# Optimization experiments

Measured on AMD Instinct MI355X. Metric: run time of the kernel, lower is better.

## Reference

```python
import jax, jax.numpy as jnp
import numpy as np

B, D, O, E = 8192, 1024, 1024, 8

def setup_inputs() -> dict:
    key = jax.random.key(0)
    ks = jax.random.split(key, 5)
    s = 1.0 / np.sqrt(D)
    return {
        "x": jax.random.normal(ks[0], (B, D), dtype=jnp.float32),
        "Wg": jax.random.uniform(ks[1], (D, E), jnp.float32, -s, s),
        "bg": jax.random.uniform(ks[2], (E,), jnp.float32, -s, s),
        "We": jax.random.uniform(ks[3], (E, D, O), jnp.float32, -s, s),
        "be": jax.random.uniform(ks[4], (E, O), jnp.float32, -s, s),
    }

def reference(x, Wg, bg, We, be):
    # gating: [B, E], softmax over experts (dim=1)
    gates = jax.nn.softmax(x @ Wg + bg, axis=1)
    # dense expert outputs: [B, E, O] (single batched GEMM over all experts)
    expert_out = jnp.einsum('bd,edo->beo', x, We) + be[None, :, :]
    # softmax-weighted combine (bmm of [B,1,E] @ [B,E,O] -> [B,O])
    return jnp.einsum('be,beo->bo', gates, expert_out)
```

## Files before the change

### kernel.cpp

```cpp
#include <hip/hip_runtime.h>
#include <hip/hip_bf16.h>
#include <stdint.h>

#define B_SZ 8192
#define D_SZ 1024
#define O_SZ 1024
#define E_SZ 8

typedef __bf16 bf16_t;
typedef __bf16 bf16x8 __attribute__((ext_vector_type(8)));
typedef __bf16 bf16x4 __attribute__((ext_vector_type(4)));
typedef float  f32x4  __attribute__((ext_vector_type(4)));

__global__ __launch_bounds__(256) void gating_kernel(
    const float* __restrict__ x, const float* __restrict__ Wg,
    const float* __restrict__ bg, float* __restrict__ gates) {
  const int w = threadIdx.x >> 6, lane = threadIdx.x & 63;
  const int b = blockIdx.x * 4 + w;
  const float* xr = x + (size_t)b * D_SZ;
  float acc[8];
#pragma unroll
  for (int e = 0; e < 8; ++e) acc[e] = 0.f;
  for (int it = 0; it < 16; ++it) {
    int d = it * 64 + lane;
    float xv = xr[d];
    const float4* wr = (const float4*)(Wg + d * 8);
    float4 w0 = wr[0], w1 = wr[1];
    acc[0] += xv * w0.x; acc[1] += xv * w0.y;
    acc[2] += xv * w0.z; acc[3] += xv * w0.w;
    acc[4] += xv * w1.x; acc[5] += xv * w1.y;
    acc[6] += xv * w1.z; acc[7] += xv * w1.w;
  }
#pragma unroll
  for (int off = 32; off >= 1; off >>= 1) {
#pragma unroll
    for (int e = 0; e < 8; ++e) acc[e] += __shfl_xor(acc[e], off, 64);
  }
  if (lane == 0) {
#pragma unroll
    for (int e = 0; e < 8; ++e) acc[e] += bg[e];
    float m = acc[0];
#pragma unroll
    for (int e = 1; e < 8; ++e) m = fmaxf(m, acc[e]);
    float s = 0.f, ex[8];
#pragma unroll
    for (int e = 0; e < 8; ++e) { ex[e] = __expf(acc[e] - m); s += ex[e]; }
    float inv = 1.0f / s;
    float* gr = gates + (size_t)b * 8;
#pragma unroll
    for (int e = 0; e < 8; ++e) gr[e] = ex[e] * inv;
  }
}

__global__ __launch_bounds__(256) void cvt_x_kernel(
    const float* __restrict__ x, bf16_t* __restrict__ xb) {
  size_t i = (size_t)blockIdx.x * 256 + threadIdx.x;
  float4 v = ((const float4*)x)[i];
  bf16x4 o;
  o[0] = (bf16_t)v.x; o[1] = (bf16_t)v.y; o[2] = (bf16_t)v.z; o[3] = (bf16_t)v.w;
  ((bf16x4*)xb)[i] = o;
}

__global__ __launch_bounds__(256) void transpose_we(
    const float* __restrict__ We, bf16_t* __restrict__ WeT) {
  __shared__ float tile[64][65];
  const int e = blockIdx.z;
  const int d0 = blockIdx.y * 64, o0 = blockIdx.x * 64;
  const int tx = threadIdx.x & 63, ty = threadIdx.x >> 6;
  const float* src = We + (size_t)e * D_SZ * O_SZ;
#pragma unroll
  for (int i = 0; i < 16; ++i) {
    int d = ty + i * 4;
    tile[d][tx] = src[(size_t)(d0 + d) * O_SZ + o0 + tx];
  }
  __syncthreads();
  bf16_t* dst = WeT + (size_t)e * O_SZ * D_SZ;
#pragma unroll
  for (int i = 0; i < 16; ++i) {
    int o = ty + i * 4;
    dst[(size_t)(o0 + o) * D_SZ + d0 + tx] = (bf16_t)tile[tx][o];
  }
}

__device__ __forceinline__ void gload_lds16(const bf16_t* g, char* l) {
  __builtin_amdgcn_global_load_lds(
      (const __attribute__((address_space(1))) void*)g,
      (__attribute__((address_space(3))) void*)l, 16, 0, 0);
}

__global__ __launch_bounds__(256, 2) void moe_gemm(
    const bf16_t* __restrict__ xb,
    const bf16_t* __restrict__ wet,
    const float* __restrict__ gates,
    const float* __restrict__ be,
    float* __restrict__ out)
{
  __shared__ bf16_t lA[128 * 32];
  __shared__ bf16_t lB[128 * 32];
  __shared__ float  lG[128 * 8];

  const int tid = threadIdx.x;
  const int b0 = blockIdx.y * 128;
  const int o0 = blockIdx.x * 128;

  {
    const float* gsrc = gates + (size_t)b0 * 8;
#pragma unroll
    for (int i = 0; i < 4; ++i) lG[tid + 256 * i] = gsrc[tid + 256 * i];
  }

  const int w = tid >> 6;
  const int lane = tid & 63;
  const int wm = (w >> 1) * 64;
  const int wn = (w & 1) * 64;
  const int m16 = lane & 15;
  const int q = lane >> 4;

  const int gi0 = tid, gi1 = tid + 256;
  const int ar0 = gi0 >> 2, ac0 = (((gi0 & 3) ^ ((gi0 >> 3) & 3)) * 8);
  const int ar1 = gi1 >> 2, ac1 = (((gi1 & 3) ^ ((gi1 >> 3) & 3)) * 8);
  char* lA0 = (char*)lA + w * 64 * 16;
  char* lA1 = (char*)lA + (256 + w * 64) * 16;
  char* lB0 = (char*)lB + w * 64 * 16;
  char* lB1 = (char*)lB + (256 + w * 64) * 16;

  const bf16_t* Abase = xb + (size_t)b0 * D_SZ;

  f32x4 outAcc[4][4];
#pragma unroll
  for (int i = 0; i < 4; ++i)
#pragma unroll
    for (int j = 0; j < 4; ++j) outAcc[i][j] = f32x4{0.f, 0.f, 0.f, 0.f};

  for (int e = 0; e < E_SZ; ++e) {
    const bf16_t* Bbase = wet + ((size_t)e * O_SZ + o0) * D_SZ;
    f32x4 acc[4][4];
#pragma unroll
    for (int i = 0; i < 4; ++i)
#pragma unroll
      for (int j = 0; j < 4; ++j) acc[i][j] = f32x4{0.f, 0.f, 0.f, 0.f};

    for (int kt = 0; kt < D_SZ / 32; ++kt) {
      const int kc = kt * 32;
      __syncthreads();
      gload_lds16(Abase + (size_t)ar0 * D_SZ + kc + ac0, lA0);
      gload_lds16(Abase + (size_t)ar1 * D_SZ + kc + ac1, lA1);
      gload_lds16(Bbase + (size_t)ar0 * D_SZ + kc + ac0, lB0);
      gload_lds16(Bbase + (size_t)ar1 * D_SZ + kc + ac1, lB1);
      __syncthreads();

      bf16x8 af[4], bf[4];
#pragma unroll
      for (int i = 0; i < 4; ++i) {
        int r = wm + i * 16 + m16;
        int pg = (q ^ ((r >> 1) & 3)) * 8;
        af[i] = *(const bf16x8*)&lA[r * 32 + pg];
      }
#pragma unroll
      for (int j = 0; j < 4; ++j) {
        int r = wn + j * 16 + m16;
        int pg = (q ^ ((r >> 1) & 3)) * 8;
        bf[j] = *(const bf16x8*)&lB[r * 32 + pg];
      }
#pragma unroll
      for (int i = 0; i < 4; ++i)
#pragma unroll
        for (int j = 0; j < 4; ++j)
          acc[i][j] = __builtin_amdgcn_mfma_f32_16x16x32_bf16(
              af[i], bf[j], acc[i][j], 0, 0, 0);
    }

#pragma unroll
    for (int j = 0; j < 4; ++j) {
      float bec = be[e * O_SZ + o0 + wn + j * 16 + m16];
#pragma unroll
      for (int i = 0; i < 4; ++i) {
#pragma unroll
        for (int rg = 0; rg < 4; ++rg) {
          float gv = lG[(wm + i * 16 + q * 4 + rg) * 8 + e];
          outAcc[i][j][rg] += gv * (acc[i][j][rg] + bec);
        }
      }
    }
  }

#pragma unroll
  for (int i = 0; i < 4; ++i)
#pragma unroll
    for (int rg = 0; rg < 4; ++rg) {
      float* orow = out + (size_t)(b0 + wm + i * 16 + q * 4 + rg) * O_SZ
                    + o0 + wn + m16;
#pragma unroll
      for (int j = 0; j < 4; ++j) orow[j * 16] = outAcc[i][j][rg];
    }
}

extern "C" void kernel_launch(void* const* d_in, const int* in_sizes, int n_in,
                              void* d_out, int out_size, void* d_ws, size_t ws_size,
                              hipStream_t stream) {
  const float* x  = (const float*)d_in[0];
  const float* Wg = (const float*)d_in[1];
  const float* bg = (const float*)d_in[2];
  const float* We = (const float*)d_in[3];
  const float* be = (const float*)d_in[4];
  float* out = (float*)d_out;

  char* ws = (char*)d_ws;
  float*  gates = (float*)ws;
  bf16_t* xb    = (bf16_t*)(ws + (1 << 18));
  bf16_t* wet   = (bf16_t*)(ws + (1 << 18) + (1 << 24));

  gating_kernel<<<B_SZ / 4, 256, 0, stream>>>(x, Wg, bg, gates);
  cvt_x_kernel<<<(B_SZ * D_SZ) / (4 * 256), 256, 0, stream>>>(x, xb);
  transpose_we<<<dim3(O_SZ / 64, D_SZ / 64, E_SZ), 256, 0, stream>>>(We, wet);
  moe_gemm<<<dim3(O_SZ / 128, B_SZ / 128), 256, 0, stream>>>(xb, wet, gates, be, out);
}
```

Before: 300.7 us.

## Split expert loop across two grid slices and fuse x conversion into gating

The expert loop in the MoE GEMM is split over a third grid dimension of two, so each block handles four experts and writes a partial result. A combine kernel then adds the partials. This doubles the block count (512 to 1024) to fill more compute units, at the cost of an extra 32MB write plus a read-add pass. Separately, the bf16 conversion of x is fused into the gating kernel so x is read once, which also removes one launch.

```diff
diff --git a/kernel.cpp b/kernel.cpp
--- a/kernel.cpp
+++ b/kernel.cpp
@@ -12,24 +12,35 @@
 typedef __bf16 bf16x4 __attribute__((ext_vector_type(4)));
 typedef float  f32x4  __attribute__((ext_vector_type(4)));
 
-__global__ __launch_bounds__(256) void gating_kernel(
+__global__ __launch_bounds__(256) void gating_cvt_kernel(
     const float* __restrict__ x, const float* __restrict__ Wg,
-    const float* __restrict__ bg, float* __restrict__ gates) {
+    const float* __restrict__ bg, float* __restrict__ gates,
+    bf16_t* __restrict__ xb) {
   const int w = threadIdx.x >> 6, lane = threadIdx.x & 63;
   const int b = blockIdx.x * 4 + w;
   const float* xr = x + (size_t)b * D_SZ;
+  bf16_t* xbr = xb + (size_t)b * D_SZ;
   float acc[8];
 #pragma unroll
   for (int e = 0; e < 8; ++e) acc[e] = 0.f;
-  for (int it = 0; it < 16; ++it) {
-    int d = it * 64 + lane;
-    float xv = xr[d];
-    const float4* wr = (const float4*)(Wg + d * 8);
-    float4 w0 = wr[0], w1 = wr[1];
-    acc[0] += xv * w0.x; acc[1] += xv * w0.y;
-    acc[2] += xv * w0.z; acc[3] += xv * w0.w;
-    acc[4] += xv * w1.x; acc[5] += xv * w1.y;
-    acc[6] += xv * w1.z; acc[7] += xv * w1.w;
+#pragma unroll
+  for (int it = 0; it < 4; ++it) {
+    const int d = it * 256 + lane * 4;
+    float4 xv = *(const float4*)(xr + d);
+    bf16x4 ov;
+    ov[0] = (bf16_t)xv.x; ov[1] = (bf16_t)xv.y;
+    ov[2] = (bf16_t)xv.z; ov[3] = (bf16_t)xv.w;
+    *(bf16x4*)(xbr + d) = ov;
+    const float xs[4] = {xv.x, xv.y, xv.z, xv.w};
+#pragma unroll
+    for (int j = 0; j < 4; ++j) {
+      const float4* wr = (const float4*)(Wg + (size_t)(d + j) * 8);
+      float4 w0 = wr[0], w1 = wr[1];
+      acc[0] += xs[j] * w0.x; acc[1] += xs[j] * w0.y;
+      acc[2] += xs[j] * w0.z; acc[3] += xs[j] * w0.w;
+      acc[4] += xs[j] * w1.x; acc[5] += xs[j] * w1.y;
+      acc[6] += xs[j] * w1.z; acc[7] += xs[j] * w1.w;
+    }
   }
 #pragma unroll
   for (int off = 32; off >= 1; off >>= 1) {
@@ -50,15 +61,6 @@
 #pragma unroll
     for (int e = 0; e < 8; ++e) gr[e] = ex[e] * inv;
   }
-}
-
-__global__ __launch_bounds__(256) void cvt_x_kernel(
-    const float* __restrict__ x, bf16_t* __restrict__ xb) {
-  size_t i = (size_t)blockIdx.x * 256 + threadIdx.x;
-  float4 v = ((const float4*)x)[i];
-  bf16x4 o;
-  o[0] = (bf16_t)v.x; o[1] = (bf16_t)v.y; o[2] = (bf16_t)v.z; o[3] = (bf16_t)v.w;
-  ((bf16x4*)xb)[i] = o;
 }
 
 __global__ __launch_bounds__(256) void transpose_we(
@@ -93,7 +95,8 @@
     const bf16_t* __restrict__ wet,
     const float* __restrict__ gates,
     const float* __restrict__ be,
-    float* __restrict__ out)
+    float* __restrict__ out,
+    float* __restrict__ part1)
 {
   __shared__ bf16_t lA[128 * 32];
   __shared__ bf16_t lB[128 * 32];
@@ -102,6 +105,10 @@
   const int tid = threadIdx.x;
   const int b0 = blockIdx.y * 128;
   const int o0 = blockIdx.x * 128;
+  const int ngrp = gridDim.z;
+  const int ne = E_SZ / ngrp;
+  const int e0 = blockIdx.z * ne;
+  float* __restrict__ dst = blockIdx.z ? part1 : out;
 
   {
     const float* gsrc = gates + (size_t)b0 * 8;
@@ -132,7 +139,8 @@
 #pragma unroll
     for (int j = 0; j < 4; ++j) outAcc[i][j] = f32x4{0.f, 0.f, 0.f, 0.f};
 
-  for (int e = 0; e < E_SZ; ++e) {
+  for (int ei = 0; ei < ne; ++ei) {
+    const int e = e0 + ei;
     const bf16_t* Bbase = wet + ((size_t)e * O_SZ + o0) * D_SZ;
     f32x4 acc[4][4];
 #pragma unroll
@@ -149,7 +157,7 @@
       gload_lds16(Bbase + (size_t)ar1 * D_SZ + kc + ac1, lB1);
       __syncthreads();
 
-      bf16x8 af[4], bf[4];
+      bf16x8 af[4], bfr[4];
 #pragma unroll
       for (int i = 0; i < 4; ++i) {
         int r = wm + i * 16 + m16;
@@ -160,14 +168,14 @@
       for (int j = 0; j < 4; ++j) {
         int r = wn + j * 16 + m16;
         int pg = (q ^ ((r >> 1) & 3)) * 8;
-        bf[j] = *(const bf16x8*)&lB[r * 32 + pg];
+        bfr[j] = *(const bf16x8*)&lB[r * 32 + pg];
       }
 #pragma unroll
       for (int i = 0; i < 4; ++i)
 #pragma unroll
         for (int j = 0; j < 4; ++j)
           acc[i][j] = __builtin_amdgcn_mfma_f32_16x16x32_bf16(
-              af[i], bf[j], acc[i][j], 0, 0, 0);
+              af[i], bfr[j], acc[i][j], 0, 0, 0);
     }
 
 #pragma unroll
@@ -188,11 +196,20 @@
   for (int i = 0; i < 4; ++i)
 #pragma unroll
     for (int rg = 0; rg < 4; ++rg) {
-      float* orow = out + (size_t)(b0 + wm + i * 16 + q * 4 + rg) * O_SZ
+      float* orow = dst + (size_t)(b0 + wm + i * 16 + q * 4 + rg) * O_SZ
                     + o0 + wn + m16;
 #pragma unroll
       for (int j = 0; j < 4; ++j) orow[j * 16] = outAcc[i][j][rg];
     }
+}
+
+__global__ __launch_bounds__(256) void combine_kernel(
+    float* __restrict__ out, const float* __restrict__ p1) {
+  size_t i = (size_t)blockIdx.x * 256 + threadIdx.x;
+  float4 a = ((const float4*)out)[i];
+  float4 b = ((const float4*)p1)[i];
+  a.x += b.x; a.y += b.y; a.z += b.z; a.w += b.w;
+  ((float4*)out)[i] = a;
 }
 
 extern "C" void kernel_launch(void* const* d_in, const int* in_sizes, int n_in,
@@ -209,9 +226,20 @@
   float*  gates = (float*)ws;
   bf16_t* xb    = (bf16_t*)(ws + (1 << 18));
   bf16_t* wet   = (bf16_t*)(ws + (1 << 18) + (1 << 24));
-
-  gating_kernel<<<B_SZ / 4, 256, 0, stream>>>(x, Wg, bg, gates);
-  cvt_x_kernel<<<(B_SZ * D_SZ) / (4 * 256), 256, 0, stream>>>(x, xb);
+  float*  p1    = (float*)(ws + (1 << 18) + 2 * (size_t)(1 << 24));
+
+  const size_t need = (size_t)(1 << 18) + 2 * (size_t)(1 << 24)
+                    + (size_t)B_SZ * O_SZ * sizeof(float);
+  const bool split = ws_size >= need;
+
+  gating_cvt_kernel<<<B_SZ / 4, 256, 0, stream>>>(x, Wg, bg, gates, xb);
   transpose_we<<<dim3(O_SZ / 64, D_SZ / 64, E_SZ), 256, 0, stream>>>(We, wet);
-  moe_gemm<<<dim3(O_SZ / 128, B_SZ / 128), 256, 0, stream>>>(xb, wet, gates, be, out);
-}
+  if (split) {
+    moe_gemm<<<dim3(O_SZ / 128, B_SZ / 128, 2), 256, 0, stream>>>(
+        xb, wet, gates, be, out, p1);
+    combine_kernel<<<(B_SZ * O_SZ / 4) / 256, 256, 0, stream>>>(out, p1);
+  } else {
+    moe_gemm<<<dim3(O_SZ / 128, B_SZ / 128, 1), 256, 0, stream>>>(
+        xb, wet, gates, be, out, p1);
+  }
+}
```

Result: slower. 333.2 us (+10.8%).

## Fuse gating, x conversion and We transpose into one prep kernel

Applied to the files above, without the earlier changes.

Merges the three preprocessing kernels into a single launch that splits its blocks between gating-plus-bf16-conversion of x and transposing/converting We. The gating path reads x once with float4 loads and reuses it for the bf16 store, removing a second full read of x. The transpose now uses float4 loads and bf16x8 stores. This cuts launch overhead and redundant traffic, but the two block roles now share one shared-memory footprint, and the transpose's tile reads with a large stride may cause LDS bank conflicts.

```diff
diff --git a/kernel.cpp b/kernel.cpp
--- a/kernel.cpp
+++ b/kernel.cpp
@@ -12,73 +12,91 @@
 typedef __bf16 bf16x4 __attribute__((ext_vector_type(4)));
 typedef float  f32x4  __attribute__((ext_vector_type(4)));
 
-__global__ __launch_bounds__(256) void gating_kernel(
+__global__ __launch_bounds__(256) void prep_kernel(
     const float* __restrict__ x, const float* __restrict__ Wg,
-    const float* __restrict__ bg, float* __restrict__ gates) {
-  const int w = threadIdx.x >> 6, lane = threadIdx.x & 63;
-  const int b = blockIdx.x * 4 + w;
-  const float* xr = x + (size_t)b * D_SZ;
-  float acc[8];
-#pragma unroll
-  for (int e = 0; e < 8; ++e) acc[e] = 0.f;
-  for (int it = 0; it < 16; ++it) {
-    int d = it * 64 + lane;
-    float xv = xr[d];
-    const float4* wr = (const float4*)(Wg + d * 8);
-    float4 w0 = wr[0], w1 = wr[1];
-    acc[0] += xv * w0.x; acc[1] += xv * w0.y;
-    acc[2] += xv * w0.z; acc[3] += xv * w0.w;
-    acc[4] += xv * w1.x; acc[5] += xv * w1.y;
-    acc[6] += xv * w1.z; acc[7] += xv * w1.w;
-  }
-#pragma unroll
-  for (int off = 32; off >= 1; off >>= 1) {
-#pragma unroll
-    for (int e = 0; e < 8; ++e) acc[e] += __shfl_xor(acc[e], off, 64);
-  }
-  if (lane == 0) {
-#pragma unroll
-    for (int e = 0; e < 8; ++e) acc[e] += bg[e];
-    float m = acc[0];
-#pragma unroll
-    for (int e = 1; e < 8; ++e) m = fmaxf(m, acc[e]);
-    float s = 0.f, ex[8];
-#pragma unroll
-    for (int e = 0; e < 8; ++e) { ex[e] = __expf(acc[e] - m); s += ex[e]; }
+    const float* __restrict__ bg, const float* __restrict__ We,
+    float* __restrict__ gates, bf16_t* __restrict__ xb,
+    bf16_t* __restrict__ WeT) {
+  __shared__ float tile[64][65];
+  const int tid = threadIdx.x;
+  if (blockIdx.x < 2048) {
+    const int w = tid >> 6, lane = tid & 63;
+    const int b = blockIdx.x * 4 + w;
+    const float* xr = x + (size_t)b * D_SZ;
+    float acc[8];
+#pragma unroll
+    for (int e = 0; e < 8; ++e) acc[e] = 0.f;
+    float xs[16];
+#pragma unroll
+    for (int it = 0; it < 4; ++it) {
+      const int d = it * 256 + lane * 4;
+      float4 xv = *(const float4*)(xr + d);
+      xs[it * 4 + 0] = xv.x; xs[it * 4 + 1] = xv.y;
+      xs[it * 4 + 2] = xv.z; xs[it * 4 + 3] = xv.w;
+#pragma unroll
+      for (int j = 0; j < 4; ++j) {
+        const float4* wr = (const float4*)(Wg + (size_t)(d + j) * 8);
+        float4 w0 = wr[0], w1 = wr[1];
+        float xj = xs[it * 4 + j];
+        acc[0] += xj * w0.x; acc[1] += xj * w0.y;
+        acc[2] += xj * w0.z; acc[3] += xj * w0.w;
+        acc[4] += xj * w1.x; acc[5] += xj * w1.y;
+        acc[6] += xj * w1.z; acc[7] += xj * w1.w;
+      }
+    }
+#pragma unroll
+    for (int off = 32; off >= 1; off >>= 1) {
+#pragma unroll
+      for (int e = 0; e < 8; ++e) acc[e] += __shfl_xor(acc[e], off, 64);
+    }
+    float g[8];
+#pragma unroll
+    for (int e = 0; e < 8; ++e) g[e] = acc[e] + bg[e];
+    float m = g[0];
+#pragma unroll
+    for (int e = 1; e < 8; ++e) m = fmaxf(m, g[e]);
+    float s = 0.f;
+#pragma unroll
+    for (int e = 0; e < 8; ++e) { g[e] = __expf(g[e] - m); s += g[e]; }
     float inv = 1.0f / s;
-    float* gr = gates + (size_t)b * 8;
-#pragma unroll
-    for (int e = 0; e < 8; ++e) gr[e] = ex[e] * inv;
-  }
-}
-
-__global__ __launch_bounds__(256) void cvt_x_kernel(
-    const float* __restrict__ x, bf16_t* __restrict__ xb) {
-  size_t i = (size_t)blockIdx.x * 256 + threadIdx.x;
-  float4 v = ((const float4*)x)[i];
-  bf16x4 o;
-  o[0] = (bf16_t)v.x; o[1] = (bf16_t)v.y; o[2] = (bf16_t)v.z; o[3] = (bf16_t)v.w;
-  ((bf16x4*)xb)[i] = o;
-}
-
-__global__ __launch_bounds__(256) void transpose_we(
-    const float* __restrict__ We, bf16_t* __restrict__ WeT) {
-  __shared__ float tile[64][65];
-  const int e = blockIdx.z;
-  const int d0 = blockIdx.y * 64, o0 = blockIdx.x * 64;
-  const int tx = threadIdx.x & 63, ty = threadIdx.x >> 6;
-  const float* src = We + (size_t)e * D_SZ * O_SZ;
-#pragma unroll
-  for (int i = 0; i < 16; ++i) {
-    int d = ty + i * 4;
-    tile[d][tx] = src[(size_t)(d0 + d) * O_SZ + o0 + tx];
-  }
-  __syncthreads();
-  bf16_t* dst = WeT + (size_t)e * O_SZ * D_SZ;
-#pragma unroll
-  for (int i = 0; i < 16; ++i) {
-    int o = ty + i * 4;
-    dst[(size_t)(o0 + o) * D_SZ + d0 + tx] = (bf16_t)tile[tx][o];
+    if (lane == 0) {
+      float* gr = gates + (size_t)b * 8;
+#pragma unroll
+      for (int e = 0; e < 8; ++e) gr[e] = g[e] * inv;
+    }
+    bf16_t* ar = xb + (size_t)b * D_SZ;
+#pragma unroll
+    for (int it = 0; it < 4; ++it) {
+      const int d = it * 256 + lane * 4;
+      bf16x4 ov;
+      ov[0] = (bf16_t)xs[it * 4 + 0]; ov[1] = (bf16_t)xs[it * 4 + 1];
+      ov[2] = (bf16_t)xs[it * 4 + 2]; ov[3] = (bf16_t)xs[it * 4 + 3];
+      *(bf16x4*)(ar + d) = ov;
+    }
+  } else {
+    const int tb = blockIdx.x - 2048;
+    const int e = tb >> 8, rem = tb & 255;
+    const int d0 = (rem >> 4) << 6, o0 = (rem & 15) << 6;
+    const float* src = We + (size_t)e * D_SZ * O_SZ + (size_t)d0 * O_SZ + o0;
+#pragma unroll
+    for (int p = 0; p < 4; ++p) {
+      const int d = p * 16 + (tid >> 4);
+      const int o = (tid & 15) * 4;
+      float4 v = *(const float4*)(src + (size_t)d * O_SZ + o);
+      tile[d][o] = v.x; tile[d][o + 1] = v.y;
+      tile[d][o + 2] = v.z; tile[d][o + 3] = v.w;
+    }
+    __syncthreads();
+    bf16_t* dstp = WeT + (size_t)e * O_SZ * D_SZ + (size_t)o0 * D_SZ + d0;
+#pragma unroll
+    for (int p = 0; p < 2; ++p) {
+      const int o = p * 32 + (tid >> 3);
+      const int d8 = (tid & 7) * 8;
+      bf16x8 ov;
+#pragma unroll
+      for (int k = 0; k < 8; ++k) ov[k] = (bf16_t)tile[d8 + k][o];
+      *(bf16x8*)(dstp + (size_t)o * D_SZ + d8) = ov;
+    }
   }
 }
 
@@ -149,7 +167,7 @@
       gload_lds16(Bbase + (size_t)ar1 * D_SZ + kc + ac1, lB1);
       __syncthreads();
 
-      bf16x8 af[4], bf[4];
+      bf16x8 af[4], bfr[4];
 #pragma unroll
       for (int i = 0; i < 4; ++i) {
         int r = wm + i * 16 + m16;
@@ -160,14 +178,14 @@
       for (int j = 0; j < 4; ++j) {
         int r = wn + j * 16 + m16;
         int pg = (q ^ ((r >> 1) & 3)) * 8;
-        bf[j] = *(const bf16x8*)&lB[r * 32 + pg];
+        bfr[j] = *(const bf16x8*)&lB[r * 32 + pg];
       }
 #pragma unroll
       for (int i = 0; i < 4; ++i)
 #pragma unroll
         for (int j = 0; j < 4; ++j)
           acc[i][j] = __builtin_amdgcn_mfma_f32_16x16x32_bf16(
-              af[i], bf[j], acc[i][j], 0, 0, 0);
+              af[i], bfr[j], acc[i][j], 0, 0, 0);
     }
 
 #pragma unroll
@@ -210,8 +228,7 @@
   bf16_t* xb    = (bf16_t*)(ws + (1 << 18));
   bf16_t* wet   = (bf16_t*)(ws + (1 << 18) + (1 << 24));
 
-  gating_kernel<<<B_SZ / 4, 256, 0, stream>>>(x, Wg, bg, gates);
-  cvt_x_kernel<<<(B_SZ * D_SZ) / (4 * 256), 256, 0, stream>>>(x, xb);
-  transpose_we<<<dim3(O_SZ / 64, D_SZ / 64, E_SZ), 256, 0, stream>>>(We, wet);
-  moe_gemm<<<dim3(O_SZ / 128, B_SZ / 128), 256, 0, stream>>>(xb, wet, gates, be, out);
-}
+  prep_kernel<<<4096, 256, 0, stream>>>(x, Wg, bg, We, gates, xb, wet);
+  moe_gemm<<<dim3(O_SZ / 128, B_SZ / 128), 256, 0, stream>>>(
+      xb, wet, gates, be, out);
+}
```

Result: slower. 308.5 us (+2.6%).
